# Optimization experiments

Hardware: AMD Instinct MI355X
Metric: run time of the kernel (lower is better)

Reference implementation:

```python
import jax, jax.numpy as jnp
import numpy as np

DILATIONS = (1, 3, 5)
NUM_HEADS = 2


def _conv(x, w, b, dil=1, pad=0):
    # x: [B,C,H,W], w: [O,I,kh,kw] (OIHW), 'same'-style padding = dilation for k=3
    y = jax.lax.conv_general_dilated(
        x, w, window_strides=(1, 1), padding=[(pad, pad), (pad, pad)],
        rhs_dilation=(dil, dil), dimension_numbers=('NCHW', 'OIHW', 'NCHW'))
    return y + b[None, :, None, None]


def setup_inputs() -> dict:
    key = jax.random.key(0)
    ks = jax.random.split(key, 4)
    B, Cin, H, W = 4, 256, 64, 64
    Cout = 256
    x = jax.random.normal(ks[0], (B, Cin, H, W), dtype=jnp.float32)
    # kaiming-uniform-like init scale
    q_w = jax.random.uniform(ks[1], (Cout, Cin, 3, 3), dtype=jnp.float32,
                             minval=-1.0, maxval=1.0) * np.sqrt(6.0 / (Cin * 9))
    k_w = jax.random.uniform(ks[2], (Cout, Cin, 1, 1), dtype=jnp.float32,
                             minval=-1.0, maxval=1.0) * np.sqrt(6.0 / Cin)
    v_w = jax.random.uniform(ks[3], (Cout, Cin, 1, 1), dtype=jnp.float32,
                             minval=-1.0, maxval=1.0) * np.sqrt(6.0 / Cin)
    q_b = jnp.zeros((Cout,), jnp.float32)
    k_b = jnp.zeros((Cout,), jnp.float32)
    v_b = jnp.zeros((Cout,), jnp.float32)
    return {"x": x, "q_w": q_w, "q_b": q_b, "k_w": k_w, "k_b": k_b,
            "v_w": v_w, "v_b": v_b}


def reference(x, q_w, q_b, k_w, k_b, v_w, v_b):
    B, C, H, W = x.shape
    Cout = q_w.shape[0]
    hd = Cout // NUM_HEADS  # head_dim
    # ds_conv2d: sum of SiLU(dilated conv) over dilations 1,3,5 (padding=dilation)
    q = sum(jax.nn.silu(_conv(x, q_w, q_b, dil=d, pad=d)) for d in DILATIONS)
    k = _conv(x, k_w, k_b)
    v = _conv(x, v_w, v_b)
    N = H * W
    # [B, heads, head_dim, N]
    q = q.reshape(B, NUM_HEADS, hd, N)
    k = k.reshape(B, NUM_HEADS, hd, N)
    v = v.reshape(B, NUM_HEADS, hd, N)
    # energy[b,h,n,m] = sum_d q[b,h,d,n] * k[b,h,d,m]
    energy = jnp.einsum('bhdn,bhdm->bhnm', q, k)
    attn = jax.nn.softmax(energy / jnp.sqrt(jnp.float32(hd)), axis=-1)
    # out[b,h,n,d] = sum_m attn[b,h,n,m] * v[b,h,d,m]; then back to [B,C,H,W]
    out = jnp.einsum('bhnm,bhdm->bhdn', attn, v)
    return out.reshape(B, Cout, H, W)
```

## Files before the change

### kernel.cpp

```cpp
#include <hip/hip_runtime.h>
#include <cstdint>

typedef __attribute__((ext_vector_type(8))) _Float16 f16x8;
typedef __attribute__((ext_vector_type(4))) float f32x4;

#define DEV static __device__ __forceinline__

DEV void gld_lds16(void* lds_base, const void* gsrc) {
  __builtin_amdgcn_global_load_lds(
      (const __attribute__((address_space(1))) unsigned int*)gsrc,
      (__attribute__((address_space(3))) unsigned int*)lds_base,
      16, 0, 0);
}
DEV unsigned short f2h(float f) {
  _Float16 h = (_Float16)f;
  return __builtin_bit_cast(unsigned short, h);
}
DEV float h2f(unsigned short u) {
  _Float16 h = __builtin_bit_cast(_Float16, u);
  return (float)h;
}
DEV unsigned pk2h(float a, float b) {
  auto h2 = __builtin_amdgcn_cvt_pkrtz(a, b);
  return __builtin_bit_cast(unsigned, h2);
}
DEV float v_exp2(float x) { float r; asm("v_exp_f32 %0, %1" : "=v"(r) : "v"(x)); return r; }
DEV float v_rcp(float x) { float r; asm("v_rcp_f32 %0, %1" : "=v"(r) : "v"(x)); return r; }


__global__ __launch_bounds__(256) void k_prep_x(const float* __restrict__ x, char* __restrict__ xpad) {
  __shared__ float xs[32 * 257];
  int h = blockIdx.x, b = blockIdx.y, t = threadIdx.x;
  const float* xb = x + (size_t)b * 1048576 + h * 64;
  for (int half = 0; half < 2; half++) {
    int w0 = half * 32;
    for (int kk = 0; kk < 32; kk++) {
      int flat = kk * 256 + t;
      int ci = flat >> 5, w = flat & 31;
      xs[w * 257 + ci] = xb[ci * 4096 + w0 + w];
    }
    __syncthreads();
    for (int g = 0; g < 4; g++) {
      int w = g * 8 + (t >> 5);
      int cg = t & 31;
      float v0 = xs[w * 257 + cg * 8 + 0], v1 = xs[w * 257 + cg * 8 + 1];
      float v2 = xs[w * 257 + cg * 8 + 2], v3 = xs[w * 257 + cg * 8 + 3];
      float v4 = xs[w * 257 + cg * 8 + 4], v5 = xs[w * 257 + cg * 8 + 5];
      float v6 = xs[w * 257 + cg * 8 + 6], v7 = xs[w * 257 + cg * 8 + 7];
      uint4 pk;
      pk.x = pk2h(v0, v1);
      pk.y = pk2h(v2, v3);
      pk.z = pk2h(v4, v5);
      pk.w = pk2h(v6, v7);
      *(uint4*)(xpad + ((size_t)((b * 74 + h + 5) * 74) + w0 + w + 5) * 512 + cg * 16) = pk;
    }
    __syncthreads();
  }
}

__global__ __launch_bounds__(256) void k_prep_w(
    const float* __restrict__ qw, const float* __restrict__ kw, const float* __restrict__ vw,
    unsigned short* __restrict__ Wq, unsigned short* __restrict__ Wk, unsigned short* __restrict__ Wv) {
  int gid = blockIdx.x * 256 + threadIdx.x;
  const float* q9 = qw + (size_t)gid * 9;
#pragma unroll
  for (int tp = 0; tp < 9; tp++) Wq[tp * 65536 + gid] = f2h(q9[tp]);
  Wk[gid] = f2h(kw[gid]);
  Wv[gid] = f2h(vw[gid]);
}

__global__ __launch_bounds__(256, 2) void k_conv_kv(
    const char* __restrict__ xpad, const unsigned short* __restrict__ Wk,
    const unsigned short* __restrict__ Wv, const float* __restrict__ kb,
    const float* __restrict__ vb, unsigned short* __restrict__ K, unsigned short* __restrict__ V) {
  __shared__ char sm[32768];
  char* Xs = sm;
  char* Ws = sm + 16384;
  int t = threadIdx.x, lane = t & 63, wid = t >> 6, q4 = lane >> 4, l15 = lane & 15;
  int px0 = blockIdx.x * 128;
  int b = px0 >> 12, nn = px0 & 4095;
  int h = blockIdx.y;
  int mode = blockIdx.z;
  int co0 = h * 128;
  const char* Wsrc = (const char*)(mode ? Wv : Wk);
  int wm = wid & 1, wn = wid >> 1;
  f32x4 acc[4][4] = {};
  for (int c = 0; c < 4; c++) {
    __syncthreads();
    for (int ch = wid * 1024; ch < 16384; ch += 4096) {
      int o = ch + lane * 16;
      int r = o >> 7;
      int n = nn + r, hh = n >> 6, ww2 = n & 63;
      int col = (o & 127) ^ ((r & 7) << 4);
      gld_lds16(Xs + ch, xpad + ((size_t)((b * 74 + hh + 5) * 74) + ww2 + 5) * 512 + c * 128 + col);
    }
    for (int ch = wid * 1024; ch < 16384; ch += 4096) {
      int o = ch + lane * 16;
      int r = o >> 7;
      int col = (o & 127) ^ ((r & 7) << 4);
      gld_lds16(Ws + ch, Wsrc + (co0 + r) * 512 + c * 128 + col);
    }
    asm volatile("s_waitcnt vmcnt(0)" ::: "memory");
    __syncthreads();
    int xg = mode ? wn : wm;
    int wg = mode ? wm : wn;
#pragma unroll
    for (int kt = 0; kt < 2; kt++) {
      f16x8 xf[4], wf[4];
#pragma unroll
      for (int i = 0; i < 4; i++) {
        int rx = xg * 64 + i * 16 + l15;
        xf[i] = *(const f16x8*)(Xs + ((rx * 128 + kt * 64 + q4 * 16) ^ ((rx & 7) << 4)));
        int rw = wg * 64 + i * 16 + l15;
        wf[i] = *(const f16x8*)(Ws + ((rw * 128 + kt * 64 + q4 * 16) ^ ((rw & 7) << 4)));
      }
#pragma unroll
      for (int m = 0; m < 4; m++)
#pragma unroll
        for (int n = 0; n < 4; n++)
          acc[m][n] = mode ? __builtin_amdgcn_mfma_f32_16x16x32_f16(wf[m], xf[n], acc[m][n], 0, 0, 0)
                           : __builtin_amdgcn_mfma_f32_16x16x32_f16(xf[m], wf[n], acc[m][n], 0, 0, 0);
    }
  }
  int bh = b * 2 + h;
  if (mode == 0) {
#pragma unroll
    for (int m = 0; m < 4; m++)
#pragma unroll
      for (int n = 0; n < 4; n++) {
        int dd = wn * 64 + n * 16 + l15;
        float bias = kb[co0 + dd];
#pragma unroll
        for (int j = 0; j < 4; j++) {
          int npix = nn + wm * 64 + m * 16 + q4 * 4 + j;
          K[(size_t)(bh * 4096 + npix) * 128 + dd] = f2h(acc[m][n][j] + bias);
        }
      }
  } else {
#pragma unroll
    for (int m = 0; m < 4; m++)
#pragma unroll
      for (int j = 0; j < 4; j++) {
        int cr = wm * 64 + m * 16 + q4 * 4 + j;
        float bias = vb[co0 + cr];
#pragma unroll
        for (int n = 0; n < 4; n++) {
          int pc = nn + wn * 64 + (n >> 1) * 32 + (l15 >> 2) * 8 + (n & 1) * 4 + (l15 & 3);
          V[(size_t)(bh * 128 + cr) * 4096 + pc] = f2h(acc[m][n][j] + bias);
        }
      }
  }
}

__global__ __launch_bounds__(256, 2) void k_conv_q(
    const char* __restrict__ xpad, const unsigned short* __restrict__ Wq,
    const float* __restrict__ qb, unsigned short* __restrict__ Q) {
  extern __shared__ char sm[];
  char* Bs = sm;
  char* As = sm + 49152;
  int t = threadIdx.x, lane = t & 63, wid = t >> 6, q4 = lane >> 4, l15 = lane & 15;
  int h = blockIdx.x, b = blockIdx.y, ch2 = blockIdx.z;
  int co0 = ch2 * 128;
  int wm = wid & 1, wn = wid >> 1;
  const int dil[3] = {1, 3, 5};
  f32x4 accd[3][2][4] = {};
  for (int kh = 0; kh < 3; kh++) {
    for (int c = 0; c < 4; c++) {
      __syncthreads();
      const char* wq_base = (const char*)Wq + kh * 3 * 131072 + co0 * 512 + c * 128;
      for (int ch = wid * 1024; ch < 49152; ch += 4096) {
        int o = ch + lane * 16;
        int kw = o >> 14;
        int r = (o >> 7) & 127;
        int col = (o & 127) ^ ((r & 7) << 4);
        gld_lds16(Bs + ch, wq_base + kw * 131072 + r * 512 + col);
      }
#pragma unroll
      for (int di = 0; di < 3; di++) {
        int pr = h + (kh - 1) * dil[di] + 5;
        const char* g = xpad + (size_t)((b * 74 + pr) * 74) * 512 + c * 128;
        char* Ad = As + di * 10240;
        for (int ch = wid * 1024; ch < 9472; ch += 4096) {
          int o = ch + lane * 16;
          if (o < 9472) {
            int r = o >> 7;
            int col = (o & 127) ^ ((r & 7) << 4);
            gld_lds16(Ad + ch, g + r * 512 + col);
          }
        }
      }
      asm volatile("s_waitcnt vmcnt(0)" ::: "memory");
      __syncthreads();
#pragma unroll
      for (int di = 0; di < 3; di++) {
        int d = dil[di];
        const char* Ad = As + di * 10240;
#pragma unroll
        for (int kw = 0; kw < 3; kw++) {
          int dw = (kw - 1) * d + 5;
          f16x8 af[2][2], bf[4][2];
#pragma unroll
          for (int m = 0; m < 2; m++)
#pragma unroll
            for (int kt = 0; kt < 2; kt++) {
              int wp = wm * 32 + m * 16 + l15 + dw;
              af[m][kt] = *(const f16x8*)(Ad + ((wp * 128 + kt * 64 + q4 * 16) ^ ((wp & 7) << 4)));
            }
#pragma unroll
          for (int n = 0; n < 4; n++)
#pragma unroll
            for (int kt = 0; kt < 2; kt++) {
              int rc = wn * 64 + n * 16 + l15;
              bf[n][kt] = *(const f16x8*)(Bs + kw * 16384 + ((rc * 128 + kt * 64 + q4 * 16) ^ ((rc & 7) << 4)));
            }
#pragma unroll
          for (int m = 0; m < 2; m++)
#pragma unroll
            for (int n = 0; n < 4; n++)
#pragma unroll
              for (int kt = 0; kt < 2; kt++)
                accd[di][m][n] = __builtin_amdgcn_mfma_f32_16x16x32_f16(af[m][kt], bf[n][kt], accd[di][m][n], 0, 0, 0);
        }
      }
    }
  }
  const float LOG2E = 1.4426950408889634f;
  const float QSCALE = 0.12751879523176862f;
#pragma unroll
  for (int n = 0; n < 4; n++) {
    float bias = qb[co0 + wn * 64 + n * 16 + l15];
#pragma unroll
    for (int m = 0; m < 2; m++)
#pragma unroll
      for (int j = 0; j < 4; j++) {
        float s = 0.f;
#pragma unroll
        for (int di = 0; di < 3; di++) {
          float v = accd[di][m][n][j] + bias;
          s += v * v_rcp(1.0f + v_exp2(-v * LOG2E));
        }
        int px = wm * 32 + m * 16 + q4 * 4 + j;
        int dd = wn * 64 + n * 16 + l15;
        int npix = h * 64 + px;
        Q[((size_t)(b * 2 + ch2) * 4096 + npix) * 128 + dd] = f2h(s * QSCALE);
      }
  }
}

__global__ __launch_bounds__(256, 2) void k_attn(
    const unsigned short* __restrict__ Q, const unsigned short* __restrict__ K,
    const unsigned short* __restrict__ V, float* __restrict__ out,
    unsigned short* __restrict__ o1buf, float* __restrict__ mlbuf) {
  extern __shared__ char sm[];
  char* K0 = sm;
  char* K1 = sm + 16384;
  char* V0 = sm + 32768;
  char* V1 = sm + 49152;
  int t = threadIdx.x, lane = t & 63, wid = t >> 6, q4 = lane >> 4, l15 = lane & 15;
  int nb = blockIdx.x, bh = blockIdx.y, half = blockIdx.z;
  int b = bh >> 1, hh = bh & 1;
  int n0 = nb * 128;
  const char* Qg = (const char*)(Q + ((size_t)bh * 4096 + n0) * 128);
  const char* Kg = (const char*)(K + (size_t)bh * 4096 * 128) + half * 524288;
  const char* Vg = (const char*)(V + (size_t)bh * 128 * 4096) + half * 4096;
  f16x8 qf[2][4];
#pragma unroll
  for (int nt = 0; nt < 2; nt++)
#pragma unroll
    for (int kt = 0; kt < 4; kt++) {
      int rn = wid * 32 + nt * 16 + l15;
      qf[nt][kt] = *(const f16x8*)(Qg + (size_t)rn * 256 + kt * 64 + q4 * 16);
    }
  for (int ch = wid * 1024; ch < 16384; ch += 4096) {
    int o = ch + lane * 16;
    gld_lds16(K0 + ch, Kg + (o ^ (((o >> 8) & 15) << 4)));
  }
  for (int ch = wid * 1024; ch < 16384; ch += 4096) {
    int o = ch + lane * 16;
    int dd = o >> 7;
    int col = (o & 127) ^ ((dd & 7) << 4);
    gld_lds16(V0 + ch, Vg + dd * 8192 + col);
  }
  asm volatile("s_waitcnt vmcnt(0)" ::: "memory");
  __syncthreads();
  f32x4 Ofr[8][2] = {};
  float mrun[2] = {-3e38f, -3e38f};
  float lrun[2] = {0.f, 0.f};
  for (int it = 0; it < 32; it++) {
    char* Kc = (it & 1) ? K1 : K0;
    char* Vc = (it & 1) ? V1 : V0;
    if (it < 31) {
      char* Kn = (it & 1) ? K0 : K1;
      char* Vn = (it & 1) ? V0 : V1;
      const char* kg = Kg + (size_t)(it + 1) * 16384;
      for (int ch = wid * 1024; ch < 16384; ch += 4096) {
        int o = ch + lane * 16;
        gld_lds16(Kn + ch, kg + (o ^ (((o >> 8) & 15) << 4)));
      }
      const char* vg = Vg + (it + 1) * 128;
      for (int ch = wid * 1024; ch < 16384; ch += 4096) {
        int o = ch + lane * 16;
        int dd = o >> 7;
        int col = (o & 127) ^ ((dd & 7) << 4);
        gld_lds16(Vn + ch, vg + dd * 8192 + col);
      }
    }
    f32x4 sT[4][2] = {};
#pragma unroll
    for (int kt = 0; kt < 4; kt++) {
      f16x8 kf[4];
#pragma unroll
      for (int mt = 0; mt < 4; mt++) {
        int rm = mt * 16 + l15;
        kf[mt] = *(const f16x8*)(Kc + ((rm * 256 + kt * 64 + q4 * 16) ^ ((rm & 15) << 4)));
      }
      __builtin_amdgcn_s_setprio(1);
#pragma unroll
      for (int mt = 0; mt < 4; mt++)
#pragma unroll
        for (int nt = 0; nt < 2; nt++)
          sT[mt][nt] = __builtin_amdgcn_mfma_f32_16x16x32_f16(kf[mt], qf[nt][kt], sT[mt][nt], 0, 0, 0);
      __builtin_amdgcn_s_setprio(0);
    }
    unsigned U[2][4][2];
#pragma unroll
    for (int nt = 0; nt < 2; nt++) {
      float mx = sT[0][nt][0];
#pragma unroll
      for (int mt = 0; mt < 4; mt++)
#pragma unroll
        for (int j = 0; j < 4; j++) mx = fmaxf(mx, sT[mt][nt][j]);
      mx = fmaxf(mx, __shfl_xor(mx, 16));
      mx = fmaxf(mx, __shfl_xor(mx, 32));
      float mn = mrun[nt];
      if (!__all(mx - mn <= 8.f)) {
        mn = fmaxf(mrun[nt], mx);
        float al = v_exp2(mrun[nt] - mn);
        mrun[nt] = mn;
        lrun[nt] *= al;
#pragma unroll
        for (int dt = 0; dt < 8; dt++) Ofr[dt][nt] *= al;
      }
      float rs = 0.f;
#pragma unroll
      for (int mt = 0; mt < 4; mt++) {
        float p0 = v_exp2(sT[mt][nt][0] - mn);
        float p1 = v_exp2(sT[mt][nt][1] - mn);
        float p2 = v_exp2(sT[mt][nt][2] - mn);
        float p3 = v_exp2(sT[mt][nt][3] - mn);
        rs += (p0 + p1) + (p2 + p3);
        U[nt][mt][0] = pk2h(p0, p1);
        U[nt][mt][1] = pk2h(p2, p3);
      }
      rs += __shfl_xor(rs, 16);
      rs += __shfl_xor(rs, 32);
      lrun[nt] += rs;
    }
#pragma unroll
    for (int kt = 0; kt < 2; kt++) {
      f16x8 pf[2];
#pragma unroll
      for (int nt = 0; nt < 2; nt++) {
        uint4 fr;
        fr.x = U[nt][2 * kt][0];
        fr.y = U[nt][2 * kt][1];
        fr.z = U[nt][2 * kt + 1][0];
        fr.w = U[nt][2 * kt + 1][1];
        pf[nt] = __builtin_bit_cast(f16x8, fr);
      }
      f16x8 vf[8];
#pragma unroll
      for (int dt = 0; dt < 8; dt++) {
        int rd = dt * 16 + l15;
        vf[dt] = *(const f16x8*)(Vc + ((rd * 128 + kt * 64 + q4 * 16) ^ ((rd & 7) << 4)));
      }
      __builtin_amdgcn_s_setprio(1);
#pragma unroll
      for (int dt = 0; dt < 8; dt++)
#pragma unroll
        for (int nt = 0; nt < 2; nt++)
          Ofr[dt][nt] = __builtin_amdgcn_mfma_f32_16x16x32_f16(vf[dt], pf[nt], Ofr[dt][nt], 0, 0, 0);
      __builtin_amdgcn_s_setprio(0);
    }
    __syncthreads();
  }
  if (q4 == 0) {
#pragma unroll
    for (int nt = 0; nt < 2; nt++) {
      int n = n0 + wid * 32 + nt * 16 + l15;
      float2 ml;
      ml.x = mrun[nt];
      ml.y = lrun[nt];
      *(float2*)(mlbuf + ((size_t)(half * 8 + bh) * 4096 + n) * 2) = ml;
    }
  }
  if (half == 0) {
    float* og = out + (size_t)(b * 256 + hh * 128) * 4096 + n0 + wid * 32;
#pragma unroll
    for (int dt = 0; dt < 8; dt++)
#pragma unroll
      for (int nt = 0; nt < 2; nt++)
#pragma unroll
        for (int j = 0; j < 4; j++) {
          int dd = dt * 16 + q4 * 4 + j;
          og[(size_t)dd * 4096 + nt * 16 + l15] = Ofr[dt][nt][j];
        }
  } else {
    float li[2] = {v_rcp(lrun[0]), v_rcp(lrun[1])};
    unsigned short* og = o1buf + (size_t)bh * 128 * 4096 + n0 + wid * 32;
#pragma unroll
    for (int dt = 0; dt < 8; dt++)
#pragma unroll
      for (int nt = 0; nt < 2; nt++)
#pragma unroll
        for (int j = 0; j < 4; j++) {
          int dd = dt * 16 + q4 * 4 + j;
          og[(size_t)dd * 4096 + nt * 16 + l15] = f2h(Ofr[dt][nt][j] * li[nt]);
        }
  }
}

__global__ __launch_bounds__(256) void k_combine(
    float* __restrict__ out, const unsigned short* __restrict__ o1,
    const float* __restrict__ ml) {
  int tid = blockIdx.x * 256 + threadIdx.x;
  int n = tid & 4095, dg = (tid >> 12) & 7, bh = tid >> 15;
  float2 ml0 = *(const float2*)(ml + ((size_t)bh * 4096 + n) * 2);
  float2 ml1 = *(const float2*)(ml + ((size_t)(8 + bh) * 4096 + n) * 2);
  float ms = fmaxf(ml0.x, ml1.x);
  float a0 = v_exp2(ml0.x - ms);
  float w1 = ml1.y * v_exp2(ml1.x - ms);
  float inv = 1.f / (ml0.y * a0 + w1);
  size_t ob = ((size_t)((bh >> 1) * 256 + (bh & 1) * 128 + dg * 16)) * 4096 + n;
  size_t o1b = ((size_t)(bh * 128 + dg * 16)) * 4096 + n;
#pragma unroll 4
  for (int j = 0; j < 16; j++) {
    float v0 = out[ob + (size_t)j * 4096];
    float v1 = h2f(o1[o1b + (size_t)j * 4096]);
    out[ob + (size_t)j * 4096] = (v0 * a0 + v1 * w1) * inv;
  }
}

extern "C" void kernel_launch(void* const* d_in, const int* in_sizes, int n_in,
                              void* d_out, int out_size, void* d_ws, size_t ws_size,
                              hipStream_t stream) {
  (void)in_sizes; (void)n_in; (void)out_size;
  const float* x  = (const float*)d_in[0];
  const float* qw = (const float*)d_in[1];
  const float* qb = (const float*)d_in[2];
  const float* kw = (const float*)d_in[3];
  const float* kb = (const float*)d_in[4];
  const float* vw = (const float*)d_in[5];
  const float* vb = (const float*)d_in[6];
  char* ws = (char*)d_ws;
  if (ws_size < 37822464) return;
  char* xpad = ws;
  unsigned short* Wq = (unsigned short*)(ws + 11214848);
  unsigned short* Wk = (unsigned short*)(ws + 12394496);
  unsigned short* Wv = (unsigned short*)(ws + 12525568);
  unsigned short* Qb = (unsigned short*)(ws + 12656640);
  unsigned short* Kb = (unsigned short*)(ws + 21045248);
  unsigned short* Vb = (unsigned short*)(ws + 29433856);
  unsigned short* O1 = (unsigned short*)ws;
  float* ML = (float*)(ws + 11214848);
  hipMemsetAsync(xpad, 0, 11214848, stream);
  k_prep_x<<<dim3(64, 4), dim3(256), 0, stream>>>(x, xpad);
  k_prep_w<<<dim3(256), dim3(256), 0, stream>>>(qw, kw, vw, Wq, Wk, Wv);
  k_conv_kv<<<dim3(128, 2, 2), dim3(256), 0, stream>>>(xpad, Wk, Wv, kb, vb, Kb, Vb);
  k_conv_q<<<dim3(64, 4, 2), dim3(256), 79872, stream>>>(xpad, Wq, qb, Qb);
  k_attn<<<dim3(32, 8, 2), dim3(256), 65536, stream>>>(Qb, Kb, Vb, (float*)d_out, O1, ML);
  k_combine<<<dim3(1024), dim3(256), 0, stream>>>((float*)d_out, O1, ML);
}
```

Measured before the change: 176.7 us.

## Swizzle block order, dedupe center-row staging, load V fragments directly from global

Both the Q-conv and attention kernels now use a flattened 1-D grid with a block-index swizzle meant to group blocks that share inputs for better L2 locality. The Q-conv kernel stages only one input row when kh==1, since all three dilations read the same center row, and it hoists the weight-fragment LDS reads out of the dilation loop so they are reused across dilations. The attention kernel drops V staging in LDS and reads V fragments straight from global memory into registers each iteration. This halves the attention LDS footprint, which may allow more resident blocks, but it exposes global-load latency and raises register pressure in the inner loop.

```diff
diff --git a/kernel.cpp b/kernel.cpp
--- a/kernel.cpp
+++ b/kernel.cpp
@@ -159,7 +159,9 @@
   char* Bs = sm;
   char* As = sm + 49152;
   int t = threadIdx.x, lane = t & 63, wid = t >> 6, q4 = lane >> 4, l15 = lane & 15;
-  int h = blockIdx.x, b = blockIdx.y, ch2 = blockIdx.z;
+  int fblk = blockIdx.x;
+  int g = (fblk & 7) * 64 + (fblk >> 3);
+  int h = g & 63, b = (g >> 6) & 3, ch2 = g >> 8;
   int co0 = ch2 * 128;
   int wm = wid & 1, wn = wid >> 1;
   const int dil[3] = {1, 3, 5};
@@ -175,30 +177,38 @@
         int col = (o & 127) ^ ((r & 7) << 4);
         gld_lds16(Bs + ch, wq_base + kw * 131072 + r * 512 + col);
       }
-#pragma unroll
-      for (int di = 0; di < 3; di++) {
+      int nst = (kh == 1) ? 1 : 3;
+      for (int di = 0; di < nst; di++) {
         int pr = h + (kh - 1) * dil[di] + 5;
-        const char* g = xpad + (size_t)((b * 74 + pr) * 74) * 512 + c * 128;
+        const char* gsrc = xpad + (size_t)((b * 74 + pr) * 74) * 512 + c * 128;
         char* Ad = As + di * 10240;
         for (int ch = wid * 1024; ch < 9472; ch += 4096) {
           int o = ch + lane * 16;
           if (o < 9472) {
             int r = o >> 7;
             int col = (o & 127) ^ ((r & 7) << 4);
-            gld_lds16(Ad + ch, g + r * 512 + col);
+            gld_lds16(Ad + ch, gsrc + r * 512 + col);
           }
         }
       }
       asm volatile("s_waitcnt vmcnt(0)" ::: "memory");
       __syncthreads();
 #pragma unroll
-      for (int di = 0; di < 3; di++) {
-        int d = dil[di];
-        const char* Ad = As + di * 10240;
-#pragma unroll
-        for (int kw = 0; kw < 3; kw++) {
+      for (int kw = 0; kw < 3; kw++) {
+        f16x8 bf[4][2];
+#pragma unroll
+        for (int n = 0; n < 4; n++)
+#pragma unroll
+          for (int kt = 0; kt < 2; kt++) {
+            int rc = wn * 64 + n * 16 + l15;
+            bf[n][kt] = *(const f16x8*)(Bs + kw * 16384 + ((rc * 128 + kt * 64 + q4 * 16) ^ ((rc & 7) << 4)));
+          }
+#pragma unroll
+        for (int di = 0; di < 3; di++) {
+          int d = dil[di];
+          const char* Ad = As + (kh == 1 ? 0 : di) * 10240;
           int dw = (kw - 1) * d + 5;
-          f16x8 af[2][2], bf[4][2];
+          f16x8 af[2][2];
 #pragma unroll
           for (int m = 0; m < 2; m++)
 #pragma unroll
@@ -207,13 +217,6 @@
               af[m][kt] = *(const f16x8*)(Ad + ((wp * 128 + kt * 64 + q4 * 16) ^ ((wp & 7) << 4)));
             }
 #pragma unroll
-          for (int n = 0; n < 4; n++)
-#pragma unroll
-            for (int kt = 0; kt < 2; kt++) {
-              int rc = wn * 64 + n * 16 + l15;
-              bf[n][kt] = *(const f16x8*)(Bs + kw * 16384 + ((rc * 128 + kt * 64 + q4 * 16) ^ ((rc & 7) << 4)));
-            }
-#pragma unroll
           for (int m = 0; m < 2; m++)
 #pragma unroll
             for (int n = 0; n < 4; n++)
@@ -251,13 +254,13 @@
     const unsigned short* __restrict__ Q, const unsigned short* __restrict__ K,
     const unsigned short* __restrict__ V, float* __restrict__ out,
     unsigned short* __restrict__ o1buf, float* __restrict__ mlbuf) {
-  extern __shared__ char sm[];
+  __shared__ char sm[32768];
   char* K0 = sm;
   char* K1 = sm + 16384;
-  char* V0 = sm + 32768;
-  char* V1 = sm + 49152;
   int t = threadIdx.x, lane = t & 63, wid = t >> 6, q4 = lane >> 4, l15 = lane & 15;
-  int nb = blockIdx.x, bh = blockIdx.y, half = blockIdx.z;
+  int fblk = blockIdx.x;
+  int g = (fblk & 7) * 64 + (fblk >> 3);
+  int nb = g & 31, bh = (g >> 5) & 7, half = g >> 8;
   int b = bh >> 1, hh = bh & 1;
   int n0 = nb * 128;
   const char* Qg = (const char*)(Q + ((size_t)bh * 4096 + n0) * 128);
@@ -274,12 +277,6 @@
   for (int ch = wid * 1024; ch < 16384; ch += 4096) {
     int o = ch + lane * 16;
     gld_lds16(K0 + ch, Kg + (o ^ (((o >> 8) & 15) << 4)));
-  }
-  for (int ch = wid * 1024; ch < 16384; ch += 4096) {
-    int o = ch + lane * 16;
-    int dd = o >> 7;
-    int col = (o & 127) ^ ((dd & 7) << 4);
-    gld_lds16(V0 + ch, Vg + dd * 8192 + col);
   }
   asm volatile("s_waitcnt vmcnt(0)" ::: "memory");
   __syncthreads();
@@ -288,21 +285,20 @@
   float lrun[2] = {0.f, 0.f};
   for (int it = 0; it < 32; it++) {
     char* Kc = (it & 1) ? K1 : K0;
-    char* Vc = (it & 1) ? V1 : V0;
+    const char* vrow = Vg + (size_t)it * 128;
+    f16x8 vfA[8], vfB[8];
+#pragma unroll
+    for (int dt = 0; dt < 8; dt++) {
+      const char* p = vrow + (size_t)(dt * 16 + l15) * 8192 + q4 * 16;
+      vfA[dt] = *(const f16x8*)p;
+      vfB[dt] = *(const f16x8*)(p + 64);
+    }
     if (it < 31) {
       char* Kn = (it & 1) ? K0 : K1;
-      char* Vn = (it & 1) ? V0 : V1;
       const char* kg = Kg + (size_t)(it + 1) * 16384;
       for (int ch = wid * 1024; ch < 16384; ch += 4096) {
         int o = ch + lane * 16;
         gld_lds16(Kn + ch, kg + (o ^ (((o >> 8) & 15) << 4)));
-      }
-      const char* vg = Vg + (it + 1) * 128;
-      for (int ch = wid * 1024; ch < 16384; ch += 4096) {
-        int o = ch + lane * 16;
-        int dd = o >> 7;
-        int col = (o & 127) ^ ((dd & 7) << 4);
-        gld_lds16(Vn + ch, vg + dd * 8192 + col);
       }
     }
     f32x4 sT[4][2] = {};
@@ -368,18 +364,12 @@
         fr.w = U[nt][2 * kt + 1][1];
         pf[nt] = __builtin_bit_cast(f16x8, fr);
       }
-      f16x8 vf[8];
-#pragma unroll
-      for (int dt = 0; dt < 8; dt++) {
-        int rd = dt * 16 + l15;
-        vf[dt] = *(const f16x8*)(Vc + ((rd * 128 + kt * 64 + q4 * 16) ^ ((rd & 7) << 4)));
-      }
       __builtin_amdgcn_s_setprio(1);
 #pragma unroll
       for (int dt = 0; dt < 8; dt++)
 #pragma unroll
         for (int nt = 0; nt < 2; nt++)
-          Ofr[dt][nt] = __builtin_amdgcn_mfma_f32_16x16x32_f16(vf[dt], pf[nt], Ofr[dt][nt], 0, 0, 0);
+          Ofr[dt][nt] = __builtin_amdgcn_mfma_f32_16x16x32_f16(kt ? vfB[dt] : vfA[dt], pf[nt], Ofr[dt][nt], 0, 0, 0);
       __builtin_amdgcn_s_setprio(0);
     }
     __syncthreads();
@@ -467,7 +457,7 @@
   k_prep_x<<<dim3(64, 4), dim3(256), 0, stream>>>(x, xpad);
   k_prep_w<<<dim3(256), dim3(256), 0, stream>>>(qw, kw, vw, Wq, Wk, Wv);
   k_conv_kv<<<dim3(128, 2, 2), dim3(256), 0, stream>>>(xpad, Wk, Wv, kb, vb, Kb, Vb);
-  k_conv_q<<<dim3(64, 4, 2), dim3(256), 79872, stream>>>(xpad, Wq, qb, Qb);
-  k_attn<<<dim3(32, 8, 2), dim3(256), 65536, stream>>>(Qb, Kb, Vb, (float*)d_out, O1, ML);
+  k_conv_q<<<dim3(512), dim3(256), 79872, stream>>>(xpad, Wq, qb, Qb);
+  k_attn<<<dim3(512), dim3(256), 0, stream>>>(Qb, Kb, Vb, (float*)d_out, O1, ML);
   k_combine<<<dim3(1024), dim3(256), 0, stream>>>((float*)d_out, O1, ML);
 }
```

Measured after the change: 238.8 us. +35.2%, slower.
